# Optimization experiments

Hardware: AMD Instinct MI355X
Metric: run time of the kernel (lower is better)

## Reference

```python
import jax, jax.numpy as jnp
import numpy as np

DIM = 2048
DIM_HEAD = 64
NUM_HEADS = 32
FFN_INNER = 4 * DIM  # 8192
SCALE = DIM_HEAD ** -0.5
LN_EPS = 1e-5


def setup_inputs() -> dict:
    key = jax.random.key(0)
    k1, k2, k3 = jax.random.split(key, 3)
    B, S = 2, 2048
    in_dim = FFN_INNER * 2 + DIM_HEAD * (NUM_HEADS + 2)  # 18560
    out_in = FFN_INNER + DIM  # 10240
    return {
        "x": jax.random.normal(k1, (B, S, DIM), jnp.float32),
        "W_in": jax.random.normal(k2, (DIM, in_dim), jnp.float32) * (DIM ** -0.5),
        "W_out": jax.random.normal(k3, (out_in, DIM), jnp.float32) * (out_in ** -0.5),
        "ln_gamma": jnp.ones((DIM,), jnp.float32),
        "ln_beta": jnp.zeros((DIM,), jnp.float32),
    }


def _rotary_pos(seq, d, dtype):
    inv_freq = 1.0 / (10000.0 ** (jnp.arange(0, d, 2, dtype=jnp.float32) / d))
    freqs = jnp.arange(seq, dtype=jnp.float32)[:, None] * inv_freq[None, :]  # [s, d/2]
    pos = jnp.concatenate([freqs, freqs], axis=-1)  # [s, d]
    return pos.astype(dtype)


def _rotate_half(t):
    d = t.shape[-1] // 2
    return jnp.concatenate([-t[..., d:], t[..., :d]], axis=-1)


def _apply_rotary(pos, t):
    return t * jnp.cos(pos) + _rotate_half(t) * jnp.sin(pos)


def reference(x, W_in, W_out, ln_gamma, ln_beta):
    B, S, D = x.shape
    # LayerNorm (residual uses the NORMED x, as in the source)
    mu = jnp.mean(x, axis=-1, keepdims=True)
    var = jnp.mean(jnp.square(x - mu), axis=-1, keepdims=True)
    xn = (x - mu) / jnp.sqrt(var + LN_EPS) * ln_gamma + ln_beta

    h = jnp.einsum('bsd,df->bsf', xn, W_in)  # fused input projection
    a = NUM_HEADS * DIM_HEAD  # attn inner dim
    q = h[..., :a]
    k = h[..., a:a + DIM_HEAD]                      # [b, s, d] shared (multi-query)
    v = h[..., a + DIM_HEAD:a + 2 * DIM_HEAD]       # [b, s, d]
    ffn_input = h[..., a + 2 * DIM_HEAD:a + 2 * DIM_HEAD + FFN_INNER]

    q = q.reshape(B, S, NUM_HEADS, DIM_HEAD).transpose(0, 2, 1, 3)  # b h s d

    pos = _rotary_pos(S, DIM_HEAD, x.dtype)
    q = _apply_rotary(pos, q)
    k = _apply_rotary(pos, k)
    q = q * SCALE

    sim = jnp.einsum('bhsd,bjd->bhsj', q, k)  # [b, h, s, s]
    causal = jnp.triu(jnp.ones((S, S), bool), 1)
    neg = jnp.finfo(sim.dtype).max
    sim = jnp.where(causal, -neg, sim)
    sim = sim - jax.lax.stop_gradient(jnp.max(sim, axis=-1, keepdims=True))
    attn = jax.nn.softmax(sim, axis=-1)

    attn_out = jnp.einsum('bhij,bjd->bhid', attn, v)  # b h s d
    attn_out = attn_out.transpose(0, 2, 1, 3).reshape(B, S, a)

    concat = jnp.concatenate([attn_out, ffn_input], axis=-1)  # [b, s, ffn+dim]
    out = jnp.einsum('bsf,fd->bsd', concat, W_out)
    return out + xn
```

## Files before the change

kernel.cpp:

```cpp
#include <hip/hip_runtime.h>
#include <cstdint>

#define NB     2
#define SEQ    2048
#define DIMN   2048
#define NROWS  (NB*SEQ)
#define NHEADS 32
#define DHEAD  64
#define FFN    8192
#define HC     10368
#define WINLD  18560
#define OI     10240

typedef __bf16 bf16_t;
typedef bf16_t bf16x8 __attribute__((ext_vector_type(8)));
typedef bf16_t bf16x4 __attribute__((ext_vector_type(4)));
typedef bf16_t bf16x2 __attribute__((ext_vector_type(2)));
typedef float  f32x4  __attribute__((ext_vector_type(4)));

typedef const uint32_t __attribute__((address_space(1)))* as1p;
typedef uint32_t __attribute__((address_space(3)))* as3p;

__device__ __forceinline__ void load_lds16(const void* g, void* l) {
  __builtin_amdgcn_global_load_lds(
      reinterpret_cast<as1p>(reinterpret_cast<uintptr_t>(g)),
      reinterpret_cast<as3p>(reinterpret_cast<uintptr_t>(l)),
      16, 0, 0);
}

__global__ __launch_bounds__(256) void ln_kernel(const float* __restrict__ x,
                                                 const float* __restrict__ gamma,
                                                 const float* __restrict__ beta,
                                                 bf16_t* __restrict__ xnb)
{
  const int row = blockIdx.x;
  const int t = threadIdx.x;
  const float4* xr = (const float4*)(x + (size_t)row * DIMN);
  float4 v0 = xr[t], v1 = xr[t + 256];
  float s  = v0.x+v0.y+v0.z+v0.w + v1.x+v1.y+v1.z+v1.w;
  float ss = v0.x*v0.x+v0.y*v0.y+v0.z*v0.z+v0.w*v0.w
           + v1.x*v1.x+v1.y*v1.y+v1.z*v1.z+v1.w*v1.w;
#pragma unroll
  for (int off = 32; off; off >>= 1) { s += __shfl_xor(s, off); ss += __shfl_xor(ss, off); }
  __shared__ float red[8];
  const int w = t >> 6;
  if ((t & 63) == 0) { red[w] = s; red[w + 4] = ss; }
  __syncthreads();
  s  = red[0]+red[1]+red[2]+red[3];
  ss = red[4]+red[5]+red[6]+red[7];
  const float mu   = s * (1.f/DIMN);
  const float var  = ss * (1.f/DIMN) - mu*mu;
  const float rstd = rsqrtf(var + 1e-5f);
  const float4* g4 = (const float4*)gamma;
  const float4* b4 = (const float4*)beta;
  float4 ga0 = g4[t], ga1 = g4[t+256], be0 = b4[t], be1 = b4[t+256];
  float4 y0, y1;
  y0.x = (v0.x-mu)*rstd*ga0.x + be0.x;  y0.y = (v0.y-mu)*rstd*ga0.y + be0.y;
  y0.z = (v0.z-mu)*rstd*ga0.z + be0.z;  y0.w = (v0.w-mu)*rstd*ga0.w + be0.w;
  y1.x = (v1.x-mu)*rstd*ga1.x + be1.x;  y1.y = (v1.y-mu)*rstd*ga1.y + be1.y;
  y1.z = (v1.z-mu)*rstd*ga1.z + be1.z;  y1.w = (v1.w-mu)*rstd*ga1.w + be1.w;
  bf16_t* xo = xnb + (size_t)row * DIMN;
  bf16x4 o0 = {(bf16_t)y0.x, (bf16_t)y0.y, (bf16_t)y0.z, (bf16_t)y0.w};
  bf16x4 o1 = {(bf16_t)y1.x, (bf16_t)y1.y, (bf16_t)y1.z, (bf16_t)y1.w};
  *(bf16x4*)(xo + t*4)        = o0;
  *(bf16x4*)(xo + (t+256)*4)  = o1;
}

__global__ __launch_bounds__(256) void tcast_kernel(const float* __restrict__ in, int ld_in,
                                                    bf16_t* __restrict__ out, int out_cols)
{
  __shared__ float tile[128][33];
  const int t = threadIdx.x;
  const int ic0 = blockIdx.x * 32;
  const int ir0 = blockIdx.y * 128;
#pragma unroll
  for (int k = 0; k < 16; k++) {
    const int idx = k*256 + t, row = idx >> 5, col = idx & 31;
    tile[row][col] = in[(size_t)(ir0 + row) * ld_in + ic0 + col];
  }
  __syncthreads();
#pragma unroll
  for (int k = 0; k < 8; k++) {
    const int idx = k*256 + t, r = idx >> 6, cp = idx & 63;
    bf16x2 v = {(bf16_t)tile[cp*2][r], (bf16_t)tile[cp*2 + 1][r]};
    *(bf16x2*)&out[(size_t)(ic0 + r) * out_cols + ir0 + cp*2] = v;
  }
}

__global__ __launch_bounds__(256, 2) void gemm1_kernel(const bf16_t* __restrict__ A,
                                                       const bf16_t* __restrict__ Bt,
                                                       bf16_t* __restrict__ C)
{
  __shared__ __align__(16) bf16_t As[128*32];
  __shared__ __align__(16) bf16_t Bs[128*32];
  const int t = threadIdx.x;
  const int id = blockIdx.x;
  const int chunk = id / 288;
  const int rem = id - chunk * 288;
  const int m0 = (rem & 31) << 7;
  const int n0 = (chunk * 9 + (rem >> 5)) << 7;
  const int l = t & 63, w = t >> 6;
  const int wm = (w >> 1) << 6, wn = (w & 1) << 6;
  const int lr = l & 15, lq = l >> 4;

  f32x4 acc[4][4];
  const f32x4 z4 = {0.f, 0.f, 0.f, 0.f};
#pragma unroll
  for (int i = 0; i < 4; i++)
#pragma unroll
    for (int j = 0; j < 4; j++) acc[i][j] = z4;

  const int srow = t >> 2, scol = (t & 3) << 3;
  bf16_t* aW = As + ((t & 192) << 3);
  bf16_t* bW = Bs + ((t & 192) << 3);
  const bf16_t* ag = A  + (size_t)(m0 + srow) * DIMN + scol;
  const bf16_t* bg = Bt + (size_t)(n0 + srow) * DIMN + scol;

  for (int k0 = 0; k0 < DIMN; k0 += 32) {
    load_lds16(ag + k0,                   aW);
    load_lds16(ag + k0 + (size_t)64*DIMN, aW + 2048);
    load_lds16(bg + k0,                   bW);
    load_lds16(bg + k0 + (size_t)64*DIMN, bW + 2048);
    __syncthreads();
    bf16x8 af[4], bb[4];
#pragma unroll
    for (int mt = 0; mt < 4; mt++)
      af[mt] = *(const bf16x8*)&As[(wm + mt*16 + lr)*32 + lq*8];
#pragma unroll
    for (int nt = 0; nt < 4; nt++)
      bb[nt] = *(const bf16x8*)&Bs[(wn + nt*16 + lr)*32 + lq*8];
#pragma unroll
    for (int mt = 0; mt < 4; mt++)
#pragma unroll
      for (int nt = 0; nt < 4; nt++)
        acc[mt][nt] = __builtin_amdgcn_mfma_f32_16x16x32_bf16(af[mt], bb[nt], acc[mt][nt], 0, 0, 0);
    __syncthreads();
  }
#pragma unroll
  for (int mt = 0; mt < 4; mt++)
#pragma unroll
    for (int nt = 0; nt < 4; nt++) {
      const int rrow = m0 + wm + mt*16 + lq*4;
      const int ccol = n0 + wn + nt*16 + lr;
      bf16_t* cp = C + (size_t)rrow * HC + ccol;
#pragma unroll
      for (int r = 0; r < 4; r++)
        cp[(size_t)r * HC] = (bf16_t)acc[mt][nt][r];
    }
}

__global__ __launch_bounds__(256) void rope_kernel(bf16_t* __restrict__ H, bf16_t* __restrict__ Vt)
{
  const int row = blockIdx.x;
  const int s = row & (SEQ - 1);
  const int b = row >> 11;
  bf16_t* hr = H + (size_t)row * HC;
  const int t = threadIdx.x;
  for (int task = t; task < 1056; task += 256) {
    const int hd = task >> 5, j = task & 31;
    const int base = (hd < 32) ? hd*64 : 2048;
    const float inv = exp2f(-(float)j * 0.41524101186092437f);
    const float ang = (float)s * inv;
    float sn, cs;
    sincosf(ang, &sn, &cs);
    const float x1 = (float)hr[base + j], x2 = (float)hr[base + j + 32];
    const float sc = (hd < 32) ? 0.125f : 1.0f;
    hr[base + j]      = (bf16_t)((x1*cs - x2*sn) * sc);
    hr[base + j + 32] = (bf16_t)((x2*cs + x1*sn) * sc);
  }
  for (int d = t; d < 64; d += 256)
    Vt[(size_t)(b*64 + d) * SEQ + s] = hr[2112 + d];
}

template<int NTMAX, bool MASK>
__device__ __forceinline__ void attn_tile_body(
    const bf16_t* __restrict__ Qs, const bf16_t* __restrict__ Ks,
    const bf16_t* __restrict__ Vts, bf16_t* __restrict__ Ps,
    f32x4 (&accO)[4], float (&m_run)[4], float (&l_run)[4],
    int w, int lr, int lq, int q0, int j0)
{
  const f32x4 z4 = {0.f,0.f,0.f,0.f};
  f32x4 accS[NTMAX];
#pragma unroll
  for (int i = 0; i < NTMAX; i++) accS[i] = z4;
  bf16x8 aq[2];
#pragma unroll
  for (int kt = 0; kt < 2; kt++)
    aq[kt] = *(const bf16x8*)&Qs[(w*16 + lr)*72 + kt*32 + lq*8];
#pragma unroll
  for (int nt = 0; nt < NTMAX; nt++)
#pragma unroll
    for (int kt = 0; kt < 2; kt++) {
      bf16x8 bk = *(const bf16x8*)&Ks[(nt*16 + lr)*72 + kt*32 + lq*8];
      accS[nt] = __builtin_amdgcn_mfma_f32_16x16x32_bf16(aq[kt], bk, accS[nt], 0, 0, 0);
    }
  if (MASK) {
    const int rg0 = q0 + w*16 + lq*4;
#pragma unroll
    for (int nt = 0; nt < NTMAX; nt++) {
      const int cg = j0 + nt*16 + lr;
#pragma unroll
      for (int r = 0; r < 4; r++)
        if (cg > rg0 + r) accS[nt][r] = -3.0e38f;
    }
  }
  float al[4];
#pragma unroll
  for (int r = 0; r < 4; r++) {
    float m = accS[0][r];
#pragma unroll
    for (int nt = 1; nt < NTMAX; nt++) m = fmaxf(m, accS[nt][r]);
    m = fmaxf(m, __shfl_xor(m, 1)); m = fmaxf(m, __shfl_xor(m, 2));
    m = fmaxf(m, __shfl_xor(m, 4)); m = fmaxf(m, __shfl_xor(m, 8));
    const float nm = fmaxf(m_run[r], m);
    al[r] = __expf(m_run[r] - nm);
    m_run[r] = nm;
  }
#pragma unroll
  for (int nt = 0; nt < NTMAX; nt++)
#pragma unroll
    for (int r = 0; r < 4; r++)
      accS[nt][r] = __expf(accS[nt][r] - m_run[r]);
#pragma unroll
  for (int r = 0; r < 4; r++) {
    float sum = 0.f;
#pragma unroll
    for (int nt = 0; nt < NTMAX; nt++) sum += accS[nt][r];
    sum += __shfl_xor(sum, 1); sum += __shfl_xor(sum, 2);
    sum += __shfl_xor(sum, 4); sum += __shfl_xor(sum, 8);
    l_run[r] = l_run[r]*al[r] + sum;
  }
#pragma unroll
  for (int nt = 0; nt < 4; nt++)
#pragma unroll
    for (int r = 0; r < 4; r++) accO[nt][r] *= al[r];
#pragma unroll
  for (int nt = 0; nt < NTMAX; nt++)
#pragma unroll
    for (int r = 0; r < 4; r++)
      Ps[(w*16 + lq*4 + r)*136 + nt*16 + lr] = (bf16_t)accS[nt][r];
  __syncthreads();
#pragma unroll
  for (int kt = 0; kt < NTMAX/2; kt++) {
    bf16x8 ap = *(const bf16x8*)&Ps[(w*16 + lr)*136 + kt*32 + lq*8];
#pragma unroll
    for (int nt = 0; nt < 4; nt++) {
      bf16x8 bv = *(const bf16x8*)&Vts[(nt*16 + lr)*136 + kt*32 + lq*8];
      accO[nt] = __builtin_amdgcn_mfma_f32_16x16x32_bf16(ap, bv, accO[nt], 0, 0, 0);
    }
  }
}

__global__ __launch_bounds__(256, 2) void attn_kernel(const bf16_t* __restrict__ H,
                                                      const bf16_t* __restrict__ Vt,
                                                      bf16_t* __restrict__ AttnOut)
{
  __shared__ __align__(16) bf16_t Qs[64*72];
  __shared__ __align__(16) bf16_t Ks[128*72];
  __shared__ __align__(16) bf16_t Vts[64*136];
  __shared__ __align__(16) bf16_t Ps[64*136];
  const int t = threadIdx.x, l = t & 63, w = t >> 6, lr = l & 15, lq = l >> 4;
  const int qb = blockIdx.x, head = blockIdx.y, b = blockIdx.z;
  const int q0 = qb * 64;
  const size_t hbase = (size_t)(b * SEQ) * HC;

#pragma unroll
  for (int i = 0; i < 2; i++) {
    const int id = t + i*256, row = id >> 3, ch = (id & 7) << 3;
    bf16x8 v = *(const bf16x8*)&H[hbase + (size_t)(q0 + row) * HC + head*64 + ch];
    *(bf16x8*)&Qs[row*72 + ch] = v;
  }
  f32x4 accO[4];
  const f32x4 z4 = {0.f,0.f,0.f,0.f};
#pragma unroll
  for (int i = 0; i < 4; i++) accO[i] = z4;
  float m_run[4], l_run[4];
#pragma unroll
  for (int r = 0; r < 4; r++) { m_run[r] = -3.0e38f; l_run[r] = 0.f; }
  const int ntiles = (qb >> 1) + 1;
  __syncthreads();

  for (int tile = 0; tile < ntiles; tile++) {
    const int j0 = tile * 128;
#pragma unroll
    for (int i = 0; i < 4; i++) {
      const int id = t + i*256, row = id >> 3, ch = (id & 7) << 3;
      bf16x8 v = *(const bf16x8*)&H[hbase + (size_t)(j0 + row) * HC + 2048 + ch];
      *(bf16x8*)&Ks[row*72 + ch] = v;
    }
#pragma unroll
    for (int i = 0; i < 4; i++) {
      const int id = t + i*256, row = id >> 4, ch = (id & 15) << 3;
      bf16x8 v = *(const bf16x8*)&Vt[(size_t)(b*64 + row) * SEQ + j0 + ch];
      *(bf16x8*)&Vts[row*136 + ch] = v;
    }
    __syncthreads();
    if (tile < ntiles - 1)
      attn_tile_body<8,false>(Qs, Ks, Vts, Ps, accO, m_run, l_run, w, lr, lq, q0, j0);
    else if ((qb & 1) == 0)
      attn_tile_body<4,true >(Qs, Ks, Vts, Ps, accO, m_run, l_run, w, lr, lq, q0, j0);
    else
      attn_tile_body<8,true >(Qs, Ks, Vts, Ps, accO, m_run, l_run, w, lr, lq, q0, j0);
    __syncthreads();
  }
  float inv_l[4];
#pragma unroll
  for (int r = 0; r < 4; r++) inv_l[r] = 1.f / l_run[r];
#pragma unroll
  for (int nt = 0; nt < 4; nt++)
#pragma unroll
    for (int r = 0; r < 4; r++)
      AttnOut[(size_t)(b*SEQ + q0 + w*16 + lq*4 + r) * DIMN + head*64 + nt*16 + lr]
          = (bf16_t)(accO[nt][r] * inv_l[r]);
}

__global__ __launch_bounds__(256, 2) void gemm2_kernel(const bf16_t* __restrict__ Attn,
                                                       const bf16_t* __restrict__ H,
                                                       const bf16_t* __restrict__ Bt,
                                                       const bf16_t* __restrict__ Res,
                                                       float* __restrict__ Out)
{
  __shared__ __align__(16) bf16_t As[128*32];
  __shared__ __align__(16) bf16_t Bs[128*32];
  const int t = threadIdx.x;
  const int id = blockIdx.x;
  const int n0 = ((((id & 7) << 1) | ((id >> 3) & 1))) << 7;
  const int m0 = (id >> 4) << 7;
  const int l = t & 63, w = t >> 6;
  const int wm = (w >> 1) << 6, wn = (w & 1) << 6;
  const int lr = l & 15, lq = l >> 4;

  f32x4 acc[4][4];
  const f32x4 z4 = {0.f, 0.f, 0.f, 0.f};
#pragma unroll
  for (int i = 0; i < 4; i++)
#pragma unroll
    for (int j = 0; j < 4; j++) acc[i][j] = z4;

  const int srow = t >> 2, scol = (t & 3) << 3;
  bf16_t* aW = As + ((t & 192) << 3);
  bf16_t* bW = Bs + ((t & 192) << 3);
  const bf16_t* agA = Attn + (size_t)(m0 + srow) * DIMN + scol;
  const bf16_t* agH = H    + (size_t)(m0 + srow) * HC + 2176 + scol;
  const bf16_t* bg  = Bt   + (size_t)(n0 + srow) * OI + scol;

  for (int k0 = 0; k0 < OI; k0 += 32) {
    const bf16_t* ag; size_t rstep;
    if (k0 < DIMN) { ag = agA + k0;          rstep = (size_t)64 * DIMN; }
    else           { ag = agH + (k0 - DIMN); rstep = (size_t)64 * HC; }
    load_lds16(ag,         aW);
    load_lds16(ag + rstep, aW + 2048);
    load_lds16(bg + k0,                 bW);
    load_lds16(bg + k0 + (size_t)64*OI, bW + 2048);
    __syncthreads();
    bf16x8 af[4], bb[4];
#pragma unroll
    for (int mt = 0; mt < 4; mt++)
      af[mt] = *(const bf16x8*)&As[(wm + mt*16 + lr)*32 + lq*8];
#pragma unroll
    for (int nt = 0; nt < 4; nt++)
      bb[nt] = *(const bf16x8*)&Bs[(wn + nt*16 + lr)*32 + lq*8];
#pragma unroll
    for (int mt = 0; mt < 4; mt++)
#pragma unroll
      for (int nt = 0; nt < 4; nt++)
        acc[mt][nt] = __builtin_amdgcn_mfma_f32_16x16x32_bf16(af[mt], bb[nt], acc[mt][nt], 0, 0, 0);
    __syncthreads();
  }
#pragma unroll
  for (int mt = 0; mt < 4; mt++)
#pragma unroll
    for (int nt = 0; nt < 4; nt++) {
      const int rrow = m0 + wm + mt*16 + lq*4;
      const int ccol = n0 + wn + nt*16 + lr;
#pragma unroll
      for (int r = 0; r < 4; r++) {
        const size_t idx = (size_t)(rrow + r) * DIMN + ccol;
        Out[idx] = acc[mt][nt][r] + (float)Res[idx];
      }
    }
}

extern "C" void kernel_launch(void* const* d_in, const int* in_sizes, int n_in,
                              void* d_out, int out_size, void* d_ws, size_t ws_size,
                              hipStream_t stream)
{
  const float* x     = (const float*)d_in[0];
  const float* W_in  = (const float*)d_in[1];
  const float* W_out = (const float*)d_in[2];
  const float* gamma = (const float*)d_in[3];
  const float* beta  = (const float*)d_in[4];
  float* out = (float*)d_out;

  char* ws = (char*)d_ws;
  bf16_t* xnb   = (bf16_t*)(ws);
  bf16_t* h     = (bf16_t*)(ws + 16777216);
  bf16_t* WinT  = (bf16_t*)(ws + 101711872);
  bf16_t* WoutT = (bf16_t*)(ws + 144179200);
  bf16_t* Vt    = (bf16_t*)(ws + 186122240);
  bf16_t* attn  = (bf16_t*)(ws + 186646528);

  ln_kernel<<<NROWS, 256, 0, stream>>>(x, gamma, beta, xnb);
  tcast_kernel<<<dim3(HC/32, DIMN/128), 256, 0, stream>>>(W_in, WINLD, WinT, DIMN);
  tcast_kernel<<<dim3(DIMN/32, OI/128), 256, 0, stream>>>(W_out, DIMN, WoutT, OI);
  gemm1_kernel<<<2592, 256, 0, stream>>>(xnb, WinT, h);
  rope_kernel<<<NROWS, 256, 0, stream>>>(h, Vt);
  attn_kernel<<<dim3(SEQ/64, NHEADS, NB), 256, 0, stream>>>(h, Vt, attn);
  gemm2_kernel<<<512, 256, 0, stream>>>(attn, h, WoutT, xnb, out);
}
```

Baseline: 920.1 us.

## Replace both GEMMs with 8-wave double-buffered ping-pong MFMA kernel

Both projection GEMMs now use one templated kernel: 512 threads, 256x256 (or 128x256) tiles and BK=64 over two LDS buffers. It uses XOR-swizzled LDS layouts, per-phase staged async global-to-LDS loads, explicit vmcnt waits, and s_setprio around MFMA bursts. The aim is to overlap loads with compute and raise data reuse compared with the old single-buffered 128x128, BK=32 kernels that synchronized twice per step. In exchange it uses much more LDS per block (likely one block per CU), and gemm1's last N tile is clamped so it overlaps and rewrites some columns.

```diff
diff --git a/kernel.cpp b/kernel.cpp
--- a/kernel.cpp
+++ b/kernel.cpp
@@ -87,66 +87,170 @@
   }
 }
 
-__global__ __launch_bounds__(256, 2) void gemm1_kernel(const bf16_t* __restrict__ A,
-                                                       const bf16_t* __restrict__ Bt,
-                                                       bf16_t* __restrict__ C)
-{
-  __shared__ __align__(16) bf16_t As[128*32];
-  __shared__ __align__(16) bf16_t Bs[128*32];
+#define BW_NONE ((void)0)
+#define BW_VM   asm volatile("s_waitcnt vmcnt(%0)" :: "n"(VM))
+#define BW_V0   asm volatile("s_waitcnt vmcnt(0)")
+
+template<int BM, int BN, int KTOT, int OP>
+__global__ __launch_bounds__(512, 2) void gemm8p(
+    const bf16_t* __restrict__ A0p, const bf16_t* __restrict__ A1p,
+    const bf16_t* __restrict__ Btp, const bf16_t* __restrict__ Res,
+    bf16_t* __restrict__ Cb, float* __restrict__ Cf)
+{
+  constexpr int NT    = KTOT / 64;
+  constexpr int NP    = NT / 2;
+  constexpr int MR    = BM / 64;
+  constexpr int NRr   = BN / 128;
+  constexpr int ALPT  = BM / 128;
+  constexpr int BLPT  = BN / 128;
+  constexpr int VM    = ALPT + BLPT;
+  constexpr int AHALF = (BM/2)*64;
+  constexpr int BHALF = (BN/2)*64;
+  constexpr int ABUF  = BM*64;
+  constexpr int BUFSZ = ABUF + BN*64;
+  constexpr int BLD   = OP ? OI : DIMN;
+  constexpr int CPX   = OP ? 32 : 82;
+  __shared__ __align__(16) bf16_t lds[2*BUFSZ];
+
   const int t = threadIdx.x;
-  const int id = blockIdx.x;
-  const int chunk = id / 288;
-  const int rem = id - chunk * 288;
-  const int m0 = (rem & 31) << 7;
-  const int n0 = (chunk * 9 + (rem >> 5)) << 7;
   const int l = t & 63, w = t >> 6;
-  const int wm = (w >> 1) << 6, wn = (w & 1) << 6;
+  const int wm2 = w >> 2, wn2 = w & 3;
   const int lr = l & 15, lq = l >> 4;
 
-  f32x4 acc[4][4];
-  const f32x4 z4 = {0.f, 0.f, 0.f, 0.f};
-#pragma unroll
-  for (int i = 0; i < 4; i++)
-#pragma unroll
-    for (int j = 0; j < 4; j++) acc[i][j] = z4;
-
-  const int srow = t >> 2, scol = (t & 3) << 3;
-  bf16_t* aW = As + ((t & 192) << 3);
-  bf16_t* bW = Bs + ((t & 192) << 3);
-  const bf16_t* ag = A  + (size_t)(m0 + srow) * DIMN + scol;
-  const bf16_t* bg = Bt + (size_t)(n0 + srow) * DIMN + scol;
-
-  for (int k0 = 0; k0 < DIMN; k0 += 32) {
-    load_lds16(ag + k0,                   aW);
-    load_lds16(ag + k0 + (size_t)64*DIMN, aW + 2048);
-    load_lds16(bg + k0,                   bW);
-    load_lds16(bg + k0 + (size_t)64*DIMN, bW + 2048);
-    __syncthreads();
-    bf16x8 af[4], bb[4];
-#pragma unroll
-    for (int mt = 0; mt < 4; mt++)
-      af[mt] = *(const bf16x8*)&As[(wm + mt*16 + lr)*32 + lq*8];
-#pragma unroll
-    for (int nt = 0; nt < 4; nt++)
-      bb[nt] = *(const bf16x8*)&Bs[(wn + nt*16 + lr)*32 + lq*8];
-#pragma unroll
-    for (int mt = 0; mt < 4; mt++)
-#pragma unroll
-      for (int nt = 0; nt < 4; nt++)
-        acc[mt][nt] = __builtin_amdgcn_mfma_f32_16x16x32_bf16(af[mt], bb[nt], acc[mt][nt], 0, 0, 0);
-    __syncthreads();
-  }
-#pragma unroll
-  for (int mt = 0; mt < 4; mt++)
-#pragma unroll
-    for (int nt = 0; nt < 4; nt++) {
-      const int rrow = m0 + wm + mt*16 + lq*4;
-      const int ccol = n0 + wn + nt*16 + lr;
-      bf16_t* cp = C + (size_t)rrow * HC + ccol;
-#pragma unroll
-      for (int r = 0; r < 4; r++)
-        cp[(size_t)r * HC] = (bf16_t)acc[mt][nt][r];
-    }
+  const int id  = blockIdx.x;
+  const int swz = (id & 7) * CPX + (id >> 3);
+  int m0, n0;
+  if (OP == 0) {
+    m0 = (swz & 15) << 8;
+    n0 = (swz >> 4) << 8;
+    if (n0 > HC - 256) n0 = HC - 256;
+  } else {
+    m0 = (swz & 31) << 7;
+    n0 = (swz >> 5) << 8;
+  }
+
+  const int rsw = (w << 3) | (l >> 3);
+  const int csw = (((l & 7) ^ ((l >> 3) & 7)) << 3);
+  const int axor[2] = { ((lq ^ (lr & 7)) << 3), (((4 + lq) ^ (lr & 7)) << 3) };
+  const int arow = wm2*(BM/4) + lr;
+  const int brow = wn2*(BN/8) + lr;
+
+  auto stA = [&](int buf, int half, int kt) {
+    const int k0 = kt * 64;
+#pragma unroll
+    for (int c = 0; c < ALPT; c++) {
+      const int gr = m0 + half*(BM/2) + c*64 + rsw;
+      const bf16_t* src;
+      if (OP == 0 || k0 < DIMN) src = A0p + (size_t)gr * DIMN + k0 + csw;
+      else                      src = A1p + (size_t)gr * HC + 2176 + (k0 - DIMN) + csw;
+      load_lds16(src, lds + buf*BUFSZ + half*AHALF + c*4096 + (w << 9));
+    }
+  };
+  auto stB = [&](int buf, int half, int kt) {
+    const int k0 = kt * 64;
+#pragma unroll
+    for (int c = 0; c < BLPT; c++) {
+      const int gr = n0 + half*(BN/2) + c*64 + rsw;
+      load_lds16(Btp + (size_t)gr * BLD + k0 + csw,
+                 lds + buf*BUFSZ + ABUF + half*BHALF + c*4096 + (w << 9));
+    }
+  };
+
+  f32x4 acc[2][2][MR][NRr];
+  const f32x4 z4 = {0.f,0.f,0.f,0.f};
+#pragma unroll
+  for (int qm = 0; qm < 2; qm++)
+#pragma unroll
+    for (int qn = 0; qn < 2; qn++)
+#pragma unroll
+      for (int i = 0; i < MR; i++)
+#pragma unroll
+        for (int j = 0; j < NRr; j++) acc[qm][qn][i][j] = z4;
+
+  stA(0,0,0); stA(0,1,0); stB(0,0,0); stB(0,1,0);
+  stA(1,0,1); stB(1,0,1);
+  BW_VM;
+  __builtin_amdgcn_sched_barrier(0);
+  __builtin_amdgcn_s_barrier();
+  __builtin_amdgcn_sched_barrier(0);
+
+#define PHASE(BUF, QM, QN, STAGE, BWAIT)                                      \
+  {                                                                           \
+    bf16x8 af[MR][2], bfr[NRr][2];                                            \
+    _Pragma("unroll")                                                         \
+    for (int i_ = 0; i_ < MR; i_++)                                           \
+      _Pragma("unroll")                                                       \
+      for (int kk_ = 0; kk_ < 2; kk_++)                                       \
+        af[i_][kk_] = *(const bf16x8*)&lds[(BUF)*BUFSZ + (QM)*AHALF           \
+                        + (arow + i_*16)*64 + axor[kk_]];                     \
+    _Pragma("unroll")                                                         \
+    for (int j_ = 0; j_ < NRr; j_++)                                          \
+      _Pragma("unroll")                                                       \
+      for (int kk_ = 0; kk_ < 2; kk_++)                                       \
+        bfr[j_][kk_] = *(const bf16x8*)&lds[(BUF)*BUFSZ + ABUF + (QN)*BHALF   \
+                        + (brow + j_*16)*64 + axor[kk_]];                     \
+    STAGE;                                                                    \
+    __builtin_amdgcn_s_barrier();                                             \
+    __builtin_amdgcn_sched_barrier(0);                                        \
+    __builtin_amdgcn_s_setprio(1);                                            \
+    _Pragma("unroll")                                                         \
+    for (int i_ = 0; i_ < MR; i_++)                                           \
+      _Pragma("unroll")                                                       \
+      for (int j_ = 0; j_ < NRr; j_++)                                        \
+        _Pragma("unroll")                                                     \
+        for (int kk_ = 0; kk_ < 2; kk_++)                                     \
+          acc[QM][QN][i_][j_] = __builtin_amdgcn_mfma_f32_16x16x32_bf16(      \
+              af[i_][kk_], bfr[j_][kk_], acc[QM][QN][i_][j_], 0, 0, 0);       \
+    __builtin_amdgcn_s_setprio(0);                                            \
+    BWAIT;                                                                    \
+    __builtin_amdgcn_s_barrier();                                             \
+    __builtin_amdgcn_sched_barrier(0);                                        \
+  }
+
+  for (int it = 0; it < NP-1; it++) {
+    const int e = 2*it, o = e+1;
+    PHASE(0,0,0, stA(1,1,o),   BW_NONE)
+    PHASE(0,0,1, stB(1,1,o),   BW_NONE)
+    PHASE(0,1,0, stA(0,0,e+2), BW_NONE)
+    PHASE(0,1,1, stB(0,0,e+2), BW_VM)
+    PHASE(1,0,0, stA(0,1,e+2), BW_NONE)
+    PHASE(1,0,1, stB(0,1,e+2), BW_NONE)
+    PHASE(1,1,0, stA(1,0,o+2), BW_NONE)
+    PHASE(1,1,1, stB(1,0,o+2), BW_VM)
+  }
+  {
+    const int o = NT-1;
+    PHASE(0,0,0, stA(1,1,o), BW_NONE)
+    PHASE(0,0,1, stB(1,1,o), BW_NONE)
+    PHASE(0,1,0, BW_NONE,    BW_NONE)
+    PHASE(0,1,1, BW_NONE,    BW_V0)
+    PHASE(1,0,0, BW_NONE,    BW_NONE)
+    PHASE(1,0,1, BW_NONE,    BW_NONE)
+    PHASE(1,1,0, BW_NONE,    BW_NONE)
+    PHASE(1,1,1, BW_NONE,    BW_NONE)
+  }
+#undef PHASE
+
+#pragma unroll
+  for (int qm = 0; qm < 2; qm++)
+#pragma unroll
+    for (int qn = 0; qn < 2; qn++)
+#pragma unroll
+      for (int i = 0; i < MR; i++)
+#pragma unroll
+        for (int j = 0; j < NRr; j++) {
+          const int row = m0 + qm*(BM/2) + wm2*(BM/4) + i*16 + lq*4;
+          const int col = n0 + qn*(BN/2) + wn2*(BN/8) + j*16 + lr;
+#pragma unroll
+          for (int r = 0; r < 4; r++) {
+            if (OP == 0) {
+              Cb[(size_t)(row + r) * HC + col] = (bf16_t)acc[qm][qn][i][j][r];
+            } else {
+              const size_t idx = (size_t)(row + r) * DIMN + col;
+              Cf[idx] = acc[qm][qn][i][j][r] + (float)Res[idx];
+            }
+          }
+        }
 }
 
 __global__ __launch_bounds__(256) void rope_kernel(bf16_t* __restrict__ H, bf16_t* __restrict__ Vt)
@@ -314,73 +418,6 @@
           = (bf16_t)(accO[nt][r] * inv_l[r]);
 }
 
-__global__ __launch_bounds__(256, 2) void gemm2_kernel(const bf16_t* __restrict__ Attn,
-                                                       const bf16_t* __restrict__ H,
-                                                       const bf16_t* __restrict__ Bt,
-                                                       const bf16_t* __restrict__ Res,
-                                                       float* __restrict__ Out)
-{
-  __shared__ __align__(16) bf16_t As[128*32];
-  __shared__ __align__(16) bf16_t Bs[128*32];
-  const int t = threadIdx.x;
-  const int id = blockIdx.x;
-  const int n0 = ((((id & 7) << 1) | ((id >> 3) & 1))) << 7;
-  const int m0 = (id >> 4) << 7;
-  const int l = t & 63, w = t >> 6;
-  const int wm = (w >> 1) << 6, wn = (w & 1) << 6;
-  const int lr = l & 15, lq = l >> 4;
-
-  f32x4 acc[4][4];
-  const f32x4 z4 = {0.f, 0.f, 0.f, 0.f};
-#pragma unroll
-  for (int i = 0; i < 4; i++)
-#pragma unroll
-    for (int j = 0; j < 4; j++) acc[i][j] = z4;
-
-  const int srow = t >> 2, scol = (t & 3) << 3;
-  bf16_t* aW = As + ((t & 192) << 3);
-  bf16_t* bW = Bs + ((t & 192) << 3);
-  const bf16_t* agA = Attn + (size_t)(m0 + srow) * DIMN + scol;
-  const bf16_t* agH = H    + (size_t)(m0 + srow) * HC + 2176 + scol;
-  const bf16_t* bg  = Bt   + (size_t)(n0 + srow) * OI + scol;
-
-  for (int k0 = 0; k0 < OI; k0 += 32) {
-    const bf16_t* ag; size_t rstep;
-    if (k0 < DIMN) { ag = agA + k0;          rstep = (size_t)64 * DIMN; }
-    else           { ag = agH + (k0 - DIMN); rstep = (size_t)64 * HC; }
-    load_lds16(ag,         aW);
-    load_lds16(ag + rstep, aW + 2048);
-    load_lds16(bg + k0,                 bW);
-    load_lds16(bg + k0 + (size_t)64*OI, bW + 2048);
-    __syncthreads();
-    bf16x8 af[4], bb[4];
-#pragma unroll
-    for (int mt = 0; mt < 4; mt++)
-      af[mt] = *(const bf16x8*)&As[(wm + mt*16 + lr)*32 + lq*8];
-#pragma unroll
-    for (int nt = 0; nt < 4; nt++)
-      bb[nt] = *(const bf16x8*)&Bs[(wn + nt*16 + lr)*32 + lq*8];
-#pragma unroll
-    for (int mt = 0; mt < 4; mt++)
-#pragma unroll
-      for (int nt = 0; nt < 4; nt++)
-        acc[mt][nt] = __builtin_amdgcn_mfma_f32_16x16x32_bf16(af[mt], bb[nt], acc[mt][nt], 0, 0, 0);
-    __syncthreads();
-  }
-#pragma unroll
-  for (int mt = 0; mt < 4; mt++)
-#pragma unroll
-    for (int nt = 0; nt < 4; nt++) {
-      const int rrow = m0 + wm + mt*16 + lq*4;
-      const int ccol = n0 + wn + nt*16 + lr;
-#pragma unroll
-      for (int r = 0; r < 4; r++) {
-        const size_t idx = (size_t)(rrow + r) * DIMN + ccol;
-        Out[idx] = acc[mt][nt][r] + (float)Res[idx];
-      }
-    }
-}
-
 extern "C" void kernel_launch(void* const* d_in, const int* in_sizes, int n_in,
                               void* d_out, int out_size, void* d_ws, size_t ws_size,
                               hipStream_t stream)
@@ -403,8 +440,8 @@
   ln_kernel<<<NROWS, 256, 0, stream>>>(x, gamma, beta, xnb);
   tcast_kernel<<<dim3(HC/32, DIMN/128), 256, 0, stream>>>(W_in, WINLD, WinT, DIMN);
   tcast_kernel<<<dim3(DIMN/32, OI/128), 256, 0, stream>>>(W_out, DIMN, WoutT, OI);
-  gemm1_kernel<<<2592, 256, 0, stream>>>(xnb, WinT, h);
+  gemm8p<256,256,DIMN,0><<<656, 512, 0, stream>>>(xnb, nullptr, WinT, nullptr, h, nullptr);
   rope_kernel<<<NROWS, 256, 0, stream>>>(h, Vt);
   attn_kernel<<<dim3(SEQ/64, NHEADS, NB), 256, 0, stream>>>(h, Vt, attn);
-  gemm2_kernel<<<512, 256, 0, stream>>>(attn, h, WoutT, xnb, out);
-}
+  gemm8p<128,256,OI,1><<<256, 512, 0, stream>>>(attn, h, WoutT, xnb, nullptr, out);
+}
```

Measured after the change: 872.8 us. 5.1% less time.
